# Optimization experiments

Hardware: AMD Instinct MI355X
Metric: run time of the kernel (lower is better)

The kernel has to match this reference:

```python
import jax, jax.numpy as jnp
import numpy as np

B, V = 128, 128000


def setup_inputs() -> dict:
    key = jax.random.key(0)
    k1, k2, k3, k4, k5, k6 = jax.random.split(key, 6)
    logits = jax.random.normal(k1, (B, V), jnp.float32) * 2.0
    temperatures = 0.5 + jax.random.uniform(k2, (B,), jnp.float32)          # [0.5, 1.5)
    top_ks = jax.random.randint(k3, (B,), 1, 1025).astype(jnp.int32)        # [1, 1024]
    top_ps = 0.7 + 0.3 * jax.random.uniform(k4, (B,), jnp.float32)          # [0.7, 1.0)
    min_ps = 0.1 * jax.random.uniform(k5, (B,), jnp.float32)                # [0.0, 0.1)
    u = jax.random.uniform(k6, (B,), jnp.float32)                           # multinomial draw
    return dict(logits=logits, temperatures=temperatures, top_ks=top_ks,
                top_ps=top_ps, min_ps=min_ps, u=u)


def reference(logits, temperatures, top_ks, top_ps, min_ps, u):
    # temperature scaling + softmax (Sampler.forward, non-greedy pytorch backend path)
    probs = jax.nn.softmax(logits / temperatures[:, None], axis=-1)          # [B, V]

    # descending sort (top_k_top_p_min_p_sampling_from_probs_torch)
    idx = jnp.argsort(-probs, axis=-1)                                        # [B, V] int
    probs_sort = jnp.take_along_axis(probs, idx, axis=-1)                     # [B, V]
    csum = jnp.cumsum(probs_sort, axis=-1)                                    # [B, V]
    ranks = jnp.arange(probs.shape[-1], dtype=jnp.int32)[None, :]             # [1, V]

    # top-k: zero ranks >= top_k; top-p: zero where cumsum - p > top_p (strict)
    keep = (ranks < top_ks[:, None]) & (csum - probs_sort <= top_ps[:, None])
    ps = jnp.where(keep, probs_sort, 0.0)
    # min-p: threshold relative to the (post top-k/top-p) max prob
    thr = ps[:, 0:1] * min_ps[:, None]
    ps = jnp.where(ps < thr, 0.0, ps)

    # multinomial(num_samples=1) via inverse-CDF with external uniform u
    cdf = jnp.cumsum(ps, axis=-1)                                             # [B, V]
    target = u[:, None] * cdf[:, -1:]
    sampled = jnp.sum(cdf < target, axis=-1, keepdims=True)                   # [B, 1]
    token_ids = jnp.take_along_axis(idx.astype(jnp.int32), sampled, axis=-1)[:, 0]  # [B]

    # logprobs = log(top_p_normalize_probs_torch(probs, top_ps)).clamp(min=finfo.min)
    ps_p = jnp.where(csum - probs_sort <= top_ps[:, None], probs_sort, 0.0)
    ps_p = ps_p / jnp.sum(ps_p, axis=-1, keepdims=True)
    rows = jnp.arange(probs.shape[0])[:, None]
    full = jnp.zeros_like(probs).at[rows, idx].set(ps_p)                      # scatter back
    logprobs = jnp.maximum(jnp.log(full), jnp.finfo(probs.dtype).min)

    next_token_logprobs = jnp.take_along_axis(logprobs, token_ids[:, None].astype(jnp.int32), axis=-1)[:, 0]
    return token_ids, logprobs, next_token_logprobs
```

## Files before the change

kernel.cpp:

```cpp
#include <hip/hip_runtime.h>
#include <hip/hip_bf16.h>

#define BB 128
#define VV 128000
#define NCHH 4
#define CHH (VV / NCHH)
#define NBIN 8192
#define HPAD 16
#define CCAP 2048
#define CEXP 16.0f
static constexpr float BF16_LO = -3.3e38f;
static_assert(VV < (1 << 17), "idx must fit 17 bits");
static_assert((CHH % 8) == 0, "vector passes");

__device__ __forceinline__ unsigned int flip_f(unsigned int b) {
    return b ^ ((b & 0x80000000u) ? 0xFFFFFFFFu : 0x80000000u);
}
__device__ __forceinline__ unsigned int unflip_f(unsigned int fx) {
    return (fx >= 0x80000000u) ? (fx ^ 0x80000000u) : ~fx;
}
__device__ __forceinline__ float key_p(unsigned long long k) {
    return __uint_as_float(~(unsigned int)(k >> 17));
}
__device__ __forceinline__ int key_i(unsigned long long k) {
    return (int)(k & 0x1FFFFull);
}
__device__ __forceinline__ int key_b(unsigned long long k) {
    return 8191 - (int)(k >> 49);
}

__global__ __launch_bounds__(1024) void k_hist(
    const float* __restrict__ logits, const float* __restrict__ temps,
    unsigned long long* __restrict__ cand, int* __restrict__ cntc,
    float* __restrict__ zpart, __hip_bfloat16* __restrict__ d_out)
{
    const int row = blockIdx.y, chunk = blockIdx.x;
    const int tid = threadIdx.x;
    const int w = tid >> 6, lane = tid & 63;
    const float rT = 1.0f / temps[row];

    __shared__ __align__(16) unsigned int hist[2 * (NBIN + HPAD)];
    __shared__ float red[16];
    __shared__ unsigned int wsum[16];
    __shared__ int wcnt[16];
    __shared__ unsigned int s_t;
    __shared__ int s_n;
    unsigned long long* lbuf = (unsigned long long*)&hist[NBIN + HPAD];

    for (int j = tid; j < 2 * (NBIN + HPAD); j += 1024) hist[j] = 0;
    unsigned int* myh = hist + (lane & 1) * (NBIN + HPAD);
    __syncthreads();

    const float4* lp4 = (const float4*)(logits + (size_t)row * VV + (size_t)chunk * CHH);
    const int N4 = CHH / 4;
    float zs = 0.f;
    int i = tid;
    bool have = i < N4;
    float4 cur = have ? lp4[i] : make_float4(0.f, 0.f, 0.f, 0.f);
    while (have) {
        const int inext = i + 1024;
        const bool hnext = inext < N4;
        float4 nxt = hnext ? lp4[inext] : make_float4(0.f, 0.f, 0.f, 0.f);
        float e4[4] = {cur.x, cur.y, cur.z, cur.w};
        #pragma unroll
        for (int e = 0; e < 4; ++e) {
            atomicAdd(&myh[flip_f(__float_as_uint(e4[e])) >> 19], 1u);
            zs += __expf(fmaf(e4[e], rT, -CEXP));
        }
        cur = nxt; i = inext; have = hnext;
    }
    #pragma unroll
    for (int off = 32; off > 0; off >>= 1) zs += __shfl_down(zs, off);
    if (lane == 0) red[w] = zs;
    __syncthreads();

    for (int j = tid; j < NBIN; j += 1024) hist[j] = hist[j] + hist[NBIN + HPAD + j];
    if (tid == 0) {
        float z = 0.f;
        #pragma unroll
        for (int i2 = 0; i2 < 16; ++i2) z += red[i2];
        zpart[row * NCHH + chunk] = z;
        s_n = 0;
    }
    __syncthreads();

    unsigned int bins[8];
    {
        uint4 a0 = *(const uint4*)&hist[tid * 8], a1 = *(const uint4*)&hist[tid * 8 + 4];
        bins[0] = a0.x; bins[1] = a0.y; bins[2] = a0.z; bins[3] = a0.w;
        bins[4] = a1.x; bins[5] = a1.y; bins[6] = a1.z; bins[7] = a1.w;
    }
    unsigned int s8 = 0;
    #pragma unroll
    for (int b = 0; b < 8; ++b) s8 += bins[b];
    unsigned int v = s8;
    #pragma unroll
    for (int off = 1; off < 64; off <<= 1) {
        unsigned int o = __shfl_down(v, off);
        v += (lane + off < 64) ? o : 0u;
    }
    if (lane == 0) wsum[w] = v;
    __syncthreads();
    unsigned int above = 0;
    for (int ww = w + 1; ww < 16; ++ww) above += wsum[ww];
    const unsigned int S = v + above;
    {
        unsigned long long bge = __ballot(S >= 1024u);
        if (lane == 0) wcnt[w] = __popcll(bge);
    }
    __syncthreads();
    {
        int tc = -1;
        for (int ww = 0; ww < 16; ++ww) tc += wcnt[ww];
        if (tid == tc) {
            unsigned int acc = S - s8;
            int bsel = -1;
            #pragma unroll
            for (int b = 7; b >= 0; --b) {
                acc += bins[b];
                if (bsel < 0 && acc >= 1024u) bsel = tid * 8 + b;
            }
            s_t = ((unsigned int)bsel) << 19;
        }
    }
    __syncthreads();

    const unsigned int t = s_t;
    for (int j = tid; j < N4; j += 1024) {
        float4 vv = lp4[j];
        float e4[4] = {vv.x, vv.y, vv.z, vv.w};
        #pragma unroll
        for (int e = 0; e < 4; ++e) {
            unsigned int fx = flip_f(__float_as_uint(e4[e]));
            if (fx >= t) {
                int pos = atomicAdd(&s_n, 1);
                if (pos < CCAP)
                    lbuf[pos] = ((unsigned long long)fx << 17)
                              | (unsigned long long)(chunk * CHH + j * 4 + e);
            }
        }
    }
    __syncthreads();
    const int n = (s_n < CCAP) ? s_n : CCAP;
    if (tid == 0) cntc[row * NCHH + chunk] = n;
    unsigned long long* gc = cand + ((size_t)row * NCHH + chunk) * CCAP;
    for (int j = tid; j < n; j += 1024) gc[j] = lbuf[j];

    {
        __hip_bfloat16 hlo = __float2bfloat16(BF16_LO);
        unsigned int pat = ((unsigned int)*(unsigned short*)&hlo) * 0x10001u;
        uint4 fv = make_uint4(pat, pat, pat, pat);
        uint4* dst = (uint4*)(d_out + BB + (size_t)row * VV + (size_t)chunk * CHH);
        for (int j = tid; j < CHH / 8; j += 1024) dst[j] = fv;
    }
}

__global__ __launch_bounds__(1024) void k_row(
    const unsigned long long* __restrict__ cand, const int* __restrict__ cntc,
    const float* __restrict__ temps, const float* __restrict__ zpart,
    const int* __restrict__ top_ks, const float* __restrict__ top_ps,
    const float* __restrict__ min_ps, const float* __restrict__ u_arr,
    __hip_bfloat16* __restrict__ d_out)
{
    const int row = blockIdx.x;
    const int tid = threadIdx.x;
    const int w = tid >> 6, lane = tid & 63;
    const float top_p = top_ps[row];

    __shared__ __align__(16) unsigned int sfx[NBIN + 4];
    __shared__ __align__(16) unsigned int cnt[NBIN];
    __shared__ __align__(16) unsigned long long skey[2048];
    __shared__ __align__(16) unsigned long long srt[1024];
    __shared__ __align__(16) float pv[1024];
    __shared__ __align__(16) float cdf[1024];
    __shared__ unsigned int wsum[16];
    __shared__ int sA[16], sB[16], sC[16];
    __shared__ double sD[16];
    __shared__ int s_bsel, s_R, s_M, s_Kp;
    __shared__ float s_tgt, s_thr, s_pcut, s_logzp;

    const int nc[4] = {cntc[row * NCHH + 0], cntc[row * NCHH + 1],
                       cntc[row * NCHH + 2], cntc[row * NCHH + 3]};
    for (int j = tid; j < NBIN / 4; j += 1024)
        *(uint4*)&cnt[j * 4] = make_uint4(0, 0, 0, 0);
    __syncthreads();

    #pragma unroll
    for (int q = 0; q < NCHH; ++q) {
        const unsigned long long* cq = cand + ((size_t)row * NCHH + q) * CCAP;
        for (int j = tid; j < nc[q]; j += 1024)
            atomicAdd(&cnt[(unsigned int)(cq[j] >> 36)], 1u);
    }
    __syncthreads();

    unsigned int bins[8];
    {
        uint4 a0 = *(const uint4*)&cnt[tid * 8], a1 = *(const uint4*)&cnt[tid * 8 + 4];
        bins[0] = a0.x; bins[1] = a0.y; bins[2] = a0.z; bins[3] = a0.w;
        bins[4] = a1.x; bins[5] = a1.y; bins[6] = a1.z; bins[7] = a1.w;
    }
    unsigned int lsfx[8];
    lsfx[7] = bins[7];
    #pragma unroll
    for (int b = 6; b >= 0; --b) lsfx[b] = bins[b] + lsfx[b + 1];
    const unsigned int s8 = lsfx[0];
    unsigned int v = s8;
    #pragma unroll
    for (int off = 1; off < 64; off <<= 1) {
        unsigned int o = __shfl_down(v, off);
        v += (lane + off < 64) ? o : 0u;
    }
    if (lane == 0) wsum[w] = v;
    __syncthreads();
    unsigned int above = 0;
    for (int ww = w + 1; ww < 16; ++ww) above += wsum[ww];
    const unsigned int thr_above = (v + above) - s8;
    {
        uint4 o0 = make_uint4(thr_above + lsfx[0], thr_above + lsfx[1],
                              thr_above + lsfx[2], thr_above + lsfx[3]);
        uint4 o1 = make_uint4(thr_above + lsfx[4], thr_above + lsfx[5],
                              thr_above + lsfx[6], thr_above + lsfx[7]);
        *(uint4*)&sfx[tid * 8] = o0;
        *(uint4*)&sfx[tid * 8 + 4] = o1;
        *(uint4*)&cnt[tid * 8] = make_uint4(0, 0, 0, 0);
        *(uint4*)&cnt[tid * 8 + 4] = make_uint4(0, 0, 0, 0);
    }
    if (tid == 0) sfx[NBIN] = 0;
    __syncthreads();

    #pragma unroll
    for (int b2 = 0; b2 < 8; ++b2) {
        const int b = tid * 8 + b2;
        if (sfx[b] >= 1024u && sfx[b + 1] < 1024u) s_bsel = b;
    }
    __syncthreads();
    const int bsel = s_bsel;
    const int n = min((int)sfx[bsel], 2048);

    const float rT = 1.0f / temps[row];
    const float Z = zpart[row * NCHH + 0] + zpart[row * NCHH + 1]
                  + zpart[row * NCHH + 2] + zpart[row * NCHH + 3];
    const float invZ = 1.0f / Z;
    #pragma unroll
    for (int q = 0; q < NCHH; ++q) {
        const unsigned long long* cq = cand + ((size_t)row * NCHH + q) * CCAP;
        for (int j = tid; j < nc[q]; j += 1024) {
            unsigned long long ck = cq[j];
            unsigned int fx = (unsigned int)(ck >> 17);
            const int b = (int)(fx >> 19);
            if (b >= bsel) {
                float l = __uint_as_float(unflip_f(fx));
                float p = __expf(fmaf(l, rT, -CEXP)) * invZ;
                unsigned int off = atomicAdd(&cnt[b], 1u);
                unsigned int slot = sfx[b + 1] + off;
                if (slot < 2048u)
                    skey[slot] = (((unsigned long long)(8191 - b)) << 49)
                               | ((unsigned long long)(~__float_as_uint(p)) << 17)
                               | (ck & 0x1FFFFull);
            }
        }
    }
    __syncthreads();

    #pragma unroll
    for (int q = 0; q < 2; ++q) {
        const int s = tid + q * 1024;
        if (s < n) {
            unsigned long long k = skey[s];
            int b = key_b(k);
            int lo = (int)sfx[b + 1];
            if (lo < 1024) {
                int hi = (int)sfx[b]; if (hi > n) hi = n;
                if (hi - lo == 1) {
                    srt[lo] = k; pv[lo] = key_p(k);
                } else {
                    int r = lo;
                    for (int j = lo; j < hi; ++j) r += (skey[j] < k);
                    if (r < 1024) { srt[r] = k; pv[r] = key_p(k); }
                }
            }
        }
    }
    __syncthreads();

    if (tid == 0) {
        float s = 0.f;
        for (int j = 0; j < 1024; j += 8) {
            float4 q0 = *(const float4*)&pv[j];
            float4 q1 = *(const float4*)&pv[j + 4];
            s += q0.x; cdf[j + 0] = s;
            s += q0.y; cdf[j + 1] = s;
            s += q0.z; cdf[j + 2] = s;
            s += q0.w; cdf[j + 3] = s;
            s += q1.x; cdf[j + 4] = s;
            s += q1.y; cdf[j + 5] = s;
            s += q1.z; cdf[j + 6] = s;
            s += q1.w; cdf[j + 7] = s;
        }
        s_thr = pv[0] * min_ps[row];
    }
    __syncthreads();

    {
        float p = pv[tid];
        float a = cdf[tid] - p;
        unsigned long long bx = __ballot(a > top_p);
        unsigned long long bm = __ballot(p < s_thr);
        if (lane == 0) {
            sA[w] = bx ? (w * 64 + __builtin_ctzll(bx)) : (1 << 30);
            sB[w] = bm ? (w * 64 + __builtin_ctzll(bm)) : (1 << 30);
        }
    }
    __syncthreads();
    if (w == 0) {
        int a = (lane < 16) ? sA[lane] : (1 << 30);
        int b2 = (lane < 16) ? sB[lane] : (1 << 30);
        #pragma unroll
        for (int off = 8; off > 0; off >>= 1) {
            a = min(a, __shfl_down(a, off));
            b2 = min(b2, __shfl_down(b2, off));
        }
        if (lane == 0) { s_R = a; s_M = b2; }
    }
    __syncthreads();

    const int R = s_R;
    const int Reff = (R <= 1023) ? R : 1024;

    {
        double zc = (tid < Reff) ? (double)pv[tid] : 0.0;
        for (int off = 32; off > 0; off >>= 1) zc += __shfl_down(zc, off);
        if (lane == 0) sD[w] = zc;
    }
    __syncthreads();
    if (w == 0) {
        double z = (lane < 16) ? sD[lane] : 0.0;
        #pragma unroll
        for (int off = 8; off > 0; off >>= 1) z += __shfl_down(z, off);
        if (lane == 0) {
            float zpv;
            if (R <= 1023)               zpv = (float)z;
            else if (cdf[1023] > top_p)  zpv = (float)z;
            else                         zpv = top_p;
            s_pcut  = pv[Reff - 1];
            s_logzp = logf(zpv);

            int K = top_ks[row]; if (Reff < K) K = Reff; if (K > 1024) K = 1024;
            int Kp = (s_M < K) ? s_M : K;
            s_Kp = Kp;
            s_tgt = u_arr[row] * cdf[Kp - 1];
        }
    }
    __syncthreads();

    {
        const int Kp = s_Kp; const float tgt = s_tgt;
        bool lt = (tid < Kp) && (cdf[tid] < tgt);
        unsigned long long bc = __ballot(lt);
        if (lane == 0) sC[w] = __popcll(bc);
    }
    __syncthreads();

    {
        const float pcut = s_pcut, logzp = s_logzp;
        for (int i = tid; i < n; i += 1024) {
            unsigned long long k = skey[i];
            float p = key_p(k);
            if (p >= pcut) {
                float val = __logf(p) - logzp;
                if (!(val >= BF16_LO)) val = BF16_LO;
                d_out[BB + (size_t)row * VV + key_i(k)] = __float2bfloat16(val);
            }
        }
    }
    if (w == 0) {
        int c2 = (lane < 16) ? sC[lane] : 0;
        #pragma unroll
        for (int off = 8; off > 0; off >>= 1) c2 += __shfl_down(c2, off);
        if (lane == 0) {
            const unsigned long long ktok = srt[c2];
            const int token = key_i(ktok);
            d_out[row] = __float2bfloat16((float)token);
            float tval = __logf(key_p(ktok)) - s_logzp;
            if (!(tval >= BF16_LO)) tval = BF16_LO;
            d_out[(size_t)BB * VV + BB + row] = __float2bfloat16(tval);
        }
    }
}

extern "C" void kernel_launch(void* const* d_in, const int* in_sizes, int n_in,
                              void* d_out, int out_size, void* d_ws, size_t ws_size,
                              hipStream_t stream) {
    const float* logits = (const float*)d_in[0];
    const float* temps  = (const float*)d_in[1];
    const int*   top_ks = (const int*)d_in[2];
    const float* top_ps = (const float*)d_in[3];
    const float* min_ps = (const float*)d_in[4];
    const float* u      = (const float*)d_in[5];
    __hip_bfloat16* out = (__hip_bfloat16*)d_out;

    char* wsb = (char*)d_ws;
    unsigned long long* cand = (unsigned long long*)wsb;
    float* zpart = (float*)(wsb + (8u << 20));
    int* cntc    = (int*)(zpart + BB * NCHH);

    k_hist<<<dim3(NCHH, BB), 1024, 0, stream>>>(logits, temps, cand, cntc, zpart, out);
    k_row<<<BB, 1024, 0, stream>>>(cand, cntc, temps, zpart,
                                   top_ks, top_ps, min_ps, u, out);
}
```

Before: 151.5 us.

## Speculatively collect candidates in first pass with fixed logit threshold

During the histogram pass, every element above a fixed logit cutoff (3.3) is written straight to the global candidate buffer. The second scan of the logits runs only if the exact histogram threshold falls below that cutoff or the buffer overflows. This is meant to remove the second read of each chunk in the common case. The cutoff is tuned to the expected logit scale, and extra shared-atomic traffic is added inside the main loop. The bf16 fill of the output is also moved from k_hist into k_row, so it now runs on 128 blocks instead of 512.

After: 151.7 us. About the same (+0.1%).

```diff
diff --git a/kernel.cpp b/kernel.cpp
--- a/kernel.cpp
+++ b/kernel.cpp
@@ -9,6 +9,7 @@
 #define HPAD 16
 #define CCAP 2048
 #define CEXP 16.0f
+#define TS_LOGIT 3.3f
 static constexpr float BF16_LO = -3.3e38f;
 static_assert(VV < (1 << 17), "idx must fit 17 bits");
 static_assert((CHH % 8) == 0, "vector passes");
@@ -32,12 +33,13 @@
 __global__ __launch_bounds__(1024) void k_hist(
     const float* __restrict__ logits, const float* __restrict__ temps,
     unsigned long long* __restrict__ cand, int* __restrict__ cntc,
-    float* __restrict__ zpart, __hip_bfloat16* __restrict__ d_out)
+    float* __restrict__ zpart)
 {
     const int row = blockIdx.y, chunk = blockIdx.x;
     const int tid = threadIdx.x;
     const int w = tid >> 6, lane = tid & 63;
     const float rT = 1.0f / temps[row];
+    const unsigned int TS = (flip_f(__float_as_uint(TS_LOGIT)) >> 19) << 19;
 
     __shared__ __align__(16) unsigned int hist[2 * (NBIN + HPAD)];
     __shared__ float red[16];
@@ -45,11 +47,13 @@
     __shared__ int wcnt[16];
     __shared__ unsigned int s_t;
     __shared__ int s_n;
-    unsigned long long* lbuf = (unsigned long long*)&hist[NBIN + HPAD];
 
     for (int j = tid; j < 2 * (NBIN + HPAD); j += 1024) hist[j] = 0;
     unsigned int* myh = hist + (lane & 1) * (NBIN + HPAD);
-    __syncthreads();
+    if (tid == 0) s_n = 0;
+    __syncthreads();
+
+    unsigned long long* gc = cand + ((size_t)row * NCHH + chunk) * CCAP;
 
     const float4* lp4 = (const float4*)(logits + (size_t)row * VV + (size_t)chunk * CHH);
     const int N4 = CHH / 4;
@@ -64,8 +68,15 @@
         float e4[4] = {cur.x, cur.y, cur.z, cur.w};
         #pragma unroll
         for (int e = 0; e < 4; ++e) {
-            atomicAdd(&myh[flip_f(__float_as_uint(e4[e])) >> 19], 1u);
+            unsigned int fx = flip_f(__float_as_uint(e4[e]));
+            atomicAdd(&myh[fx >> 19], 1u);
             zs += __expf(fmaf(e4[e], rT, -CEXP));
+            if (fx >= TS) {
+                int pos = atomicAdd(&s_n, 1);
+                if (pos < CCAP)
+                    gc[pos] = ((unsigned long long)fx << 17)
+                            | (unsigned long long)(chunk * CHH + i * 4 + e);
+            }
         }
         cur = nxt; i = inext; have = hnext;
     }
@@ -80,7 +91,6 @@
         #pragma unroll
         for (int i2 = 0; i2 < 16; ++i2) z += red[i2];
         zpart[row * NCHH + chunk] = z;
-        s_n = 0;
     }
     __syncthreads();
 
@@ -125,34 +135,28 @@
     }
     __syncthreads();
 
-    const unsigned int t = s_t;
-    for (int j = tid; j < N4; j += 1024) {
-        float4 vv = lp4[j];
-        float e4[4] = {vv.x, vv.y, vv.z, vv.w};
-        #pragma unroll
-        for (int e = 0; e < 4; ++e) {
-            unsigned int fx = flip_f(__float_as_uint(e4[e]));
-            if (fx >= t) {
-                int pos = atomicAdd(&s_n, 1);
-                if (pos < CCAP)
-                    lbuf[pos] = ((unsigned long long)fx << 17)
-                              | (unsigned long long)(chunk * CHH + j * 4 + e);
-            }
-        }
-    }
-    __syncthreads();
-    const int n = (s_n < CCAP) ? s_n : CCAP;
-    if (tid == 0) cntc[row * NCHH + chunk] = n;
-    unsigned long long* gc = cand + ((size_t)row * NCHH + chunk) * CCAP;
-    for (int j = tid; j < n; j += 1024) gc[j] = lbuf[j];
-
-    {
-        __hip_bfloat16 hlo = __float2bfloat16(BF16_LO);
-        unsigned int pat = ((unsigned int)*(unsigned short*)&hlo) * 0x10001u;
-        uint4 fv = make_uint4(pat, pat, pat, pat);
-        uint4* dst = (uint4*)(d_out + BB + (size_t)row * VV + (size_t)chunk * CHH);
-        for (int j = tid; j < CHH / 8; j += 1024) dst[j] = fv;
-    }
+    const bool ok = (TS <= s_t) && (s_n <= CCAP);
+    if (!ok) {
+        if (tid == 0) s_n = 0;
+        __syncthreads();
+        const unsigned int t = s_t;
+        for (int j = tid; j < N4; j += 1024) {
+            float4 vv = lp4[j];
+            float e4[4] = {vv.x, vv.y, vv.z, vv.w};
+            #pragma unroll
+            for (int e = 0; e < 4; ++e) {
+                unsigned int fx = flip_f(__float_as_uint(e4[e]));
+                if (fx >= t) {
+                    int pos = atomicAdd(&s_n, 1);
+                    if (pos < CCAP)
+                        gc[pos] = ((unsigned long long)fx << 17)
+                                | (unsigned long long)(chunk * CHH + j * 4 + e);
+                }
+            }
+        }
+        __syncthreads();
+    }
+    if (tid == 0) cntc[row * NCHH + chunk] = (s_n < CCAP) ? s_n : CCAP;
 }
 
 __global__ __launch_bounds__(1024) void k_row(
@@ -178,6 +182,14 @@
     __shared__ double sD[16];
     __shared__ int s_bsel, s_R, s_M, s_Kp;
     __shared__ float s_tgt, s_thr, s_pcut, s_logzp;
+
+    {
+        __hip_bfloat16 hlo = __float2bfloat16(BF16_LO);
+        unsigned int pat = ((unsigned int)*(unsigned short*)&hlo) * 0x10001u;
+        uint4 fv = make_uint4(pat, pat, pat, pat);
+        uint4* dst = (uint4*)(d_out + BB + (size_t)row * VV);
+        for (int j = tid; j < VV / 8; j += 1024) dst[j] = fv;
+    }
 
     const int nc[4] = {cntc[row * NCHH + 0], cntc[row * NCHH + 1],
                        cntc[row * NCHH + 2], cntc[row * NCHH + 3]};
@@ -404,7 +416,7 @@
     float* zpart = (float*)(wsb + (8u << 20));
     int* cntc    = (int*)(zpart + BB * NCHH);
 
-    k_hist<<<dim3(NCHH, BB), 1024, 0, stream>>>(logits, temps, cand, cntc, zpart, out);
+    k_hist<<<dim3(NCHH, BB), 1024, 0, stream>>>(logits, temps, cand, cntc, zpart);
     k_row<<<BB, 1024, 0, stream>>>(cand, cntc, temps, zpart,
                                    top_ks, top_ps, min_ps, u, out);
 }
```
